# Performance work log

Measured on AMD Instinct MI355X. Metric: run time of the kernel, lower is better.

## Reference

```python
import jax, jax.numpy as jnp
import numpy as np
from jax import lax

KSIZE = 3      # match kernel
STRIDE = 1
RATE = 2       # dilation / downscale rate
FUSE_K = 3     # diagonal-fuse kernel
SCALE = 10.0   # softmax scale
FUSE = True
ESC = 1e-4     # escape_NaN, added per-element before the reduce_sum (as in torch code)


def _same_pad(x, k, s):
    # x: [C, H, W] -> zero-padded so that strided k-window 'same' extraction works
    C, H, W = x.shape
    oh, ow = -(-H // s), -(-W // s)
    ph = max(0, (oh - 1) * s + k - H)
    pw = max(0, (ow - 1) * s + k - W)
    xp = jnp.pad(x, ((0, 0), (ph // 2, ph - ph // 2), (pw // 2, pw - pw // 2)))
    return xp, oh, ow


def extract_patches(x, k, s):
    # x: [C, H, W] -> [L, C, k, k], L row-major over output grid (matches torch Unfold)
    C = x.shape[0]
    xp, oh, ow = _same_pad(x, k, s)
    cols = [xp[:, dh:dh + s * (oh - 1) + 1:s, dw:dw + s * (ow - 1) + 1:s]
            for dh in range(k) for dw in range(k)]
    p = jnp.stack(cols, 0).reshape(k, k, C, oh, ow)
    return p.transpose(3, 4, 2, 0, 1).reshape(oh * ow, C, k, k)


def fuse_diag(x):
    # conv with eye(FUSE_K) kernel, 'same' padding: sum of diagonal shifts
    A, B = x.shape
    pt = (FUSE_K - 1) // 2
    pb = FUSE_K - 1 - pt
    xp = jnp.pad(x, ((pt, pb), (pt, pb)))
    out = xp[0:A, 0:B]
    for d in range(1, FUSE_K):
        out = out + xp[d:d + A, d:d + B]
    return out


def _forward(f, b, mask):
    B, C, H, W = f.shape
    kernel = 2 * RATE
    # mask -> mm gate over background patches (shared across batch: torch uses m[0])
    mask_s = mask[0][:, ::4 * RATE, ::4 * RATE]           # [1, H/r, W/r] nearest downsample
    m = extract_patches(mask_s, KSIZE, STRIDE)            # [L, 1, k, k]
    mm = (jnp.mean(m, axis=(1, 2, 3)) == 0.0).astype(f.dtype)[:, None, None]  # [L,1,1]

    def single(fi, bi):
        # raw patches from full-res background for reconstruction: [Lb, C, 2r, 2r]
        raw_w = extract_patches(bi, kernel, RATE * STRIDE)
        # nearest 1/rate downsample
        fs = fi[:, ::RATE, ::RATE]
        bs = bi[:, ::RATE, ::RATE]
        bh, bw = bs.shape[1], bs.shape[2]
        fh, fw = fs.shape[1], fs.shape[2]
        Lb, Lf = bh * bw, fh * fw
        # match patches from downsampled background, L2-normalized per patch
        w = extract_patches(bs, KSIZE, STRIDE)                      # [Lb, C, 3, 3]
        denom = jnp.sqrt(jnp.sum(w * w + ESC, axis=(1, 2, 3), keepdims=True))
        wn = (w / denom).reshape(Lb, -1)                            # [Lb, C*9]
        # correlation = conv of fs with wn filters = patch GEMM
        fp = extract_patches(fs, KSIZE, 1).reshape(Lf, -1)          # [Lf, C*9]
        scores = wn @ fp.T                                          # [Lb, Lf]
        if FUSE:
            s = fuse_diag(scores)
            s = s.reshape(bh, bw, fh, fw).transpose(1, 0, 3, 2).reshape(Lb, Lf)
            s = fuse_diag(s)
            s = s.reshape(bw, bh, fw, fh).transpose(1, 0, 3, 2).reshape(Lb, Lf)
            scores = s
        att = scores.reshape(Lb, fh, fw) * mm
        att = jax.nn.softmax(att * SCALE, axis=0) * mm              # softmax over patches
        # conv_transpose2d(att, raw_w, stride=rate, padding=1) / 4
        rhs = jnp.flip(raw_w, (2, 3)).transpose(1, 0, 2, 3)         # [C, Lb, 2r, 2r] OIHW
        pad = kernel - 1 - 1                                        # k - 1 - torch_padding
        out = lax.conv_general_dilated(
            att[None], rhs, window_strides=(1, 1),
            padding=[(pad, pad), (pad, pad)], lhs_dilation=(RATE, RATE),
            dimension_numbers=('NCHW', 'OIHW', 'NCHW'))[0] / 4.0    # [C, H, W]
        return out

    return jax.vmap(single)(f, b)


def setup_inputs() -> dict:
    key = jax.random.key(0)
    k1, k2 = jax.random.split(key)
    B, C, H, W = 4, 128, 96, 96
    f = jax.random.normal(k1, (B, C, H, W), jnp.float32)
    b = jax.random.normal(k2, (B, C, H, W), jnp.float32)
    mask = jnp.zeros((1, 1, 4 * H, 4 * W), jnp.float32)
    mask = mask.at[:, :, 96:288, 96:288].set(1.0)
    return {"f": f, "b": b, "mask": mask}


def reference(f, b, mask):
    return _forward(f, b, mask)
```

## Files before the change

### kernel.cpp

```cpp
#include <hip/hip_runtime.h>

typedef _Float16 half8 __attribute__((ext_vector_type(8)));
typedef float floatx4 __attribute__((ext_vector_type(4)));

#define LBF 2304
#define K1  1152
#define LDK2 2304

__device__ __forceinline__ void gll16(const _Float16* g, _Float16* l) {
    __builtin_amdgcn_global_load_lds((const __attribute__((address_space(1))) void*)g,
                                     (__attribute__((address_space(3))) void*)l, 16, 0, 0);
}

__device__ __forceinline__ int dec_kc(int s) { return (s >= 0) ? s + 1 : -s - 1; }

__global__ void stage_scan(const float* __restrict__ f, const float* __restrict__ bsrc,
                           const float* __restrict__ mask,
                           float* __restrict__ ds, int* __restrict__ pos) {
    int tid = threadIdx.x;
    if (blockIdx.x < 9216) {
        long flat = (long)blockIdx.x * 256 + tid;
        int p = flat % 2304;
        long rest = flat / 2304;
        int c = rest % 128;
        int b = (rest / 128) % 4;
        int t = rest / (128 * 4);
        int pi = p / 48, pj = p % 48;
        const float* src = t ? bsrc : f;
        ds[flat] = src[(((long)b * 128 + c) * 96 + 2 * pi) * 96 + 2 * pj];
        return;
    }
    int mmb[9], loc[9]; int s = 0;
#pragma unroll
    for (int t = 0; t < 9; t++) {
        int p = tid * 9 + t;
        int pi = p / 48, pj = p % 48;
        float sm = 0.f;
#pragma unroll
        for (int u = 0; u < 3; u++)
#pragma unroll
            for (int v = 0; v < 3; v++) {
                int y = pi - 1 + u, x = pj - 1 + v;
                if ((unsigned)y < 48u && (unsigned)x < 48u)
                    sm += mask[(8 * y) * 384 + 8 * x];
            }
        int m = (sm == 0.f) ? 1 : 0;
        mmb[t] = m; loc[t] = s; s += m;
    }
    __shared__ int sh[256];
    sh[tid] = s; __syncthreads();
    for (int off = 1; off < 256; off <<= 1) {
        int v = (tid >= off) ? sh[tid - off] : 0;
        __syncthreads();
        sh[tid] += v;
        __syncthreads();
    }
    int excl = sh[tid] - s;
#pragma unroll
    for (int t = 0; t < 9; t++) {
        int e = excl + loc[t];
        pos[tid * 9 + t] = mmb[t] ? e : (-e - 1);
    }
}

__global__ void prep_fp(const float* __restrict__ ds, _Float16* __restrict__ fp) {
    int k = blockIdx.x * 128 + threadIdx.x;
    int p = blockIdx.y;
    int b = blockIdx.z;
    int c = k / 9, r = k % 9, u = r / 3, v = r % 3;
    int pi = p / 48, pj = p % 48;
    int y = pi - 1 + u, x = pj - 1 + v;
    float val = 0.f;
    if ((unsigned)y < 48u && (unsigned)x < 48u)
        val = ds[((long)(b * 128 + c)) * 2304 + y * 48 + x];
    fp[((long)b * LBF + p) * K1 + k] = (_Float16)val;
}

__global__ void prep_wn(const float* __restrict__ ds, _Float16* __restrict__ wn) {
    int p = blockIdx.x, b = blockIdx.y;
    int tid = threadIdx.x;
    int pi = p / 48, pj = p % 48;
    const float* dsb = ds + (long)(4 + b) * 128 * 2304;
    float w[9];
    float ss = 0.f;
#pragma unroll
    for (int t = 0; t < 9; t++) {
        int k = tid + t * 128;
        int c = k / 9, r = k % 9, u = r / 3, v = r % 3;
        int y = pi - 1 + u, x = pj - 1 + v;
        float val = 0.f;
        if ((unsigned)y < 48u && (unsigned)x < 48u)
            val = dsb[(long)c * 2304 + y * 48 + x];
        w[t] = val;
        ss += val * val;
    }
    for (int m = 32; m; m >>= 1) ss += __shfl_xor(ss, m);
    __shared__ float sh[2];
    if ((tid & 63) == 0) sh[tid >> 6] = ss;
    __syncthreads();
    float denom = sqrtf(sh[0] + sh[1] + 0.1152f);
    float inv = 1.f / denom;
#pragma unroll
    for (int t = 0; t < 9; t++) {
        int k = tid + t * 128;
        wn[((long)b * LBF + p) * K1 + k] = (_Float16)(w[t] * inv);
    }
}

__global__ void prep_wtc(const float* __restrict__ bsrc, const int* __restrict__ pos,
                         _Float16* __restrict__ wtc) {
    int p = blockIdx.x * 256 + threadIdx.x;
    int c = blockIdx.y;
    int b = blockIdx.z;
    int sp = pos[p];
    long base = ((long)b * 2048 + c * 16) * LDK2;
    if (sp < 0) {
        int kc = dec_kc(pos[2303]);
        int kp = (kc + 63) & ~63;
        int mo = p + sp + 1;
        if (mo < kp - kc) {
#pragma unroll
            for (int n = 0; n < 16; n++)
                wtc[base + (long)n * LDK2 + kc + mo] = (_Float16)0.f;
        }
        return;
    }
    int pi = p / 48, pj = p % 48;
    const float* src = bsrc + ((long)b * 128 + c) * 96 * 96;
#pragma unroll
    for (int u = 0; u < 4; u++) {
        int y = 2 * pi - 1 + u;
        bool yok = (unsigned)y < 96u;
#pragma unroll
        for (int v = 0; v < 4; v++) {
            int x = 2 * pj - 1 + v;
            float val = 0.f;
            if (yok && (unsigned)x < 96u) val = src[y * 96 + x];
            wtc[base + (long)(u * 4 + v) * LDK2 + sp] = (_Float16)val;
        }
    }
}

#define REGA 8192
#define REGB 4096

__global__ __launch_bounds__(512, 2)
void gemm1_8ph(const _Float16* __restrict__ A, const _Float16* __restrict__ B,
               float* __restrict__ C) {
    extern __shared__ _Float16 smem[];
    _Float16* SA = smem;
    _Float16* SB = smem + 4 * REGA;

    int bid = blockIdx.x;
    int wg = (bid & 7) * 81 + (bid >> 3);
    int z = wg / 162; int t = wg - z * 162;
    const int m0 = (t / 18) * 256, n0 = (t % 18) * 128;

    const _Float16* gA = A + (long)z * 2304 * K1 + (long)m0 * K1;
    const _Float16* gB = B + (long)z * 2304 * K1 + (long)n0 * K1;
    float* Cb = C + (long)z * 2304 * 2304;

    const int tid = threadIdx.x;
    const int wave = tid >> 6, lane = tid & 63;
    const int lm = lane & 15, q = lane >> 4;
    const int wm = wave >> 1, wn_ = wave & 1;
    const int soff = (q ^ ((lm >> 1) & 3)) * 8;
    const int srow = lane >> 2;
    const int scol = (((lane & 3) ^ ((lane >> 3) & 3))) * 8;

    floatx4 acc[4][4] = {};

    auto stA = [&](int reg, int kcol) {
        _Float16* dst = SA + reg * REGA;
        gll16(gA + (long)(wave * 32 + srow) * K1 + kcol, dst + wave * 1024);
        gll16(gA + (long)(wave * 32 + 16 + srow) * K1 + kcol, dst + wave * 1024 + 512);
    };
    auto stB = [&](int reg, int kcol) {
        gll16(gB + (long)(wave * 16 + srow) * K1 + kcol, SB + reg * REGB + wave * 512);
    };
    auto ldA = [&](int reg, int i) -> half8 {
        return *(const half8*)&SA[reg * REGA + (wm * 64 + i * 16 + lm) * 32 + soff];
    };
    auto ldB = [&](int reg, int j) -> half8 {
        return *(const half8*)&SB[reg * REGB + (wn_ * 64 + j * 16 + lm) * 32 + soff];
    };

    stA(0, 0 + scol);  stB(0, 0 + scol);
    stA(1, 32 + scol); stB(1, 32 + scol);
    stA(2, 64 + scol); stB(2, 64 + scol);
    asm volatile("s_waitcnt vmcnt(6)" ::: "memory");
    __builtin_amdgcn_s_barrier();

    for (int k = 0; k < 18; ++k) {
        const int b = k & 1;
        const int rg0 = b * 2, rg1 = rg0 + 1, og1 = (b ^ 1) * 2 + 1;
        {
            half8 af[4], bf[4];
#pragma unroll
            for (int i = 0; i < 4; ++i) af[i] = ldA(rg0, i);
#pragma unroll
            for (int j = 0; j < 4; ++j) bf[j] = ldB(rg0, j);
            if (k + 1 < 18) { int kc = (k + 1) * 64 + 32 + scol; stA(og1, kc); stB(og1, kc); }
            asm volatile("s_waitcnt vmcnt(6)" ::: "memory");
            __builtin_amdgcn_s_barrier();
            __builtin_amdgcn_s_setprio(1);
#pragma unroll
            for (int i = 0; i < 4; ++i)
#pragma unroll
                for (int j = 0; j < 4; ++j)
                    acc[i][j] = __builtin_amdgcn_mfma_f32_16x16x32_f16(af[i], bf[j], acc[i][j], 0, 0, 0);
            __builtin_amdgcn_s_setprio(0);
            __builtin_amdgcn_s_barrier();
        }
        {
            half8 af[4], bf[4];
#pragma unroll
            for (int i = 0; i < 4; ++i) af[i] = ldA(rg1, i);
#pragma unroll
            for (int j = 0; j < 4; ++j) bf[j] = ldB(rg1, j);
            if (k + 2 < 18) { int kc = (k + 2) * 64 + scol; stA(rg0, kc); stB(rg0, kc); }
            asm volatile("s_waitcnt vmcnt(6)" ::: "memory");
            __builtin_amdgcn_s_barrier();
            __builtin_amdgcn_s_setprio(1);
#pragma unroll
            for (int i = 0; i < 4; ++i)
#pragma unroll
                for (int j = 0; j < 4; ++j)
                    acc[i][j] = __builtin_amdgcn_mfma_f32_16x16x32_f16(af[i], bf[j], acc[i][j], 0, 0, 0);
            __builtin_amdgcn_s_setprio(0);
            __builtin_amdgcn_s_barrier();
        }
    }

    const int col = n0 + wn_ * 64 + lm;
#pragma unroll
    for (int i = 0; i < 4; ++i) {
        const int row = m0 + wm * 64 + i * 16 + q * 4;
#pragma unroll
        for (int j = 0; j < 4; ++j)
#pragma unroll
            for (int r = 0; r < 4; ++r)
                Cb[(long)(row + r) * 2304 + col + j * 16] = acc[i][j][r];
    }
}

__device__ __forceinline__ void gemm_compute(const _Float16* lA, const _Float16* lB,
                                             floatx4 (&acc)[4][4],
                                             int wr, int wc, int lm, int pcp) {
    half8 af[4], bf[4];
#pragma unroll
    for (int t = 0; t < 4; t++) {
        af[t] = *(const half8*)&lA[(wr * 64 + t * 16 + lm) * 64 + pcp];
        bf[t] = *(const half8*)&lB[(wc * 64 + t * 16 + lm) * 64 + pcp];
    }
#pragma unroll
    for (int i = 0; i < 4; i++)
#pragma unroll
        for (int j = 0; j < 4; j++)
            acc[i][j] = __builtin_amdgcn_mfma_f32_16x16x32_f16(af[i], bf[j], acc[i][j], 0, 0, 0);
#pragma unroll
    for (int t = 0; t < 4; t++) {
        af[t] = *(const half8*)&lA[(wr * 64 + t * 16 + lm) * 64 + (pcp ^ 32)];
        bf[t] = *(const half8*)&lB[(wc * 64 + t * 16 + lm) * 64 + (pcp ^ 32)];
    }
#pragma unroll
    for (int i = 0; i < 4; i++)
#pragma unroll
        for (int j = 0; j < 4; j++)
            acc[i][j] = __builtin_amdgcn_mfma_f32_16x16x32_f16(af[i], bf[j], acc[i][j], 0, 0, 0);
}

__global__ __launch_bounds__(256)
void gemm_nt64(const _Float16* __restrict__ A, const _Float16* __restrict__ B,
               float* __restrict__ C, int M, int N, int ldk, int swapxy,
               const int* __restrict__ Kpos, int Kstat, long sA, long sB, long sC) {
    A += blockIdx.z * sA; B += blockIdx.z * sB; C += blockIdx.z * sC;
    int K;
    if (Kpos) { int kc = dec_kc(Kpos[0]); K = (kc + 63) & ~63; }
    else K = Kstat;
    const int tid = threadIdx.x;
    const int lane = tid & 63, wave = tid >> 6;
    const int wr = wave >> 1, wc = wave & 1;
    const int bm = swapxy ? blockIdx.x : blockIdx.y;
    const int bn = swapxy ? blockIdx.y : blockIdx.x;
    const int m0 = bm * 128, n0 = bn * 128;

    __shared__ _Float16 sm[4][128 * 64];

    floatx4 acc[4][4] = {};

    const int lm = lane & 15, q = lane >> 4;
    const int pcp = (q ^ (lm & 7)) * 8;

    const int srow8 = lane >> 3;
    const int gc = ((lane & 7) ^ srow8) * 8;
    const _Float16* gA[4]; const _Float16* gB[4];
    int dOff[4];
#pragma unroll
    for (int c = 0; c < 4; c++) {
        int r = (wave * 4 + c) * 8 + srow8;
        gA[c] = A + (long)(m0 + r) * ldk + gc;
        gB[c] = B + (long)(n0 + r) * ldk + gc;
        dOff[c] = (wave * 4 + c) * 512;
    }

    if (K > 0) {
#pragma unroll
        for (int c = 0; c < 4; c++) gll16(gA[c], &sm[0][dOff[c]]);
#pragma unroll
        for (int c = 0; c < 4; c++) gll16(gB[c], &sm[1][dOff[c]]);
        __syncthreads();
        int k0 = 0, buf = 0;
        while (true) {
            int kn = k0 + 64;
            if (kn < K) {
                const int nb = (buf ^ 1) * 2;
#pragma unroll
                for (int c = 0; c < 4; c++) gll16(gA[c] + kn, &sm[nb][dOff[c]]);
#pragma unroll
                for (int c = 0; c < 4; c++) gll16(gB[c] + kn, &sm[nb + 1][dOff[c]]);
            }
            gemm_compute(sm[buf * 2], sm[buf * 2 + 1], acc, wr, wc, lm, pcp);
            __syncthreads();
            k0 = kn; buf ^= 1;
            if (k0 >= K) break;
        }
    }

    const int col = n0 + wc * 64 + lm;
    const int rowq = q * 4;
#pragma unroll
    for (int i = 0; i < 4; i++) {
        int row = m0 + wr * 64 + i * 16 + rowq;
#pragma unroll
        for (int j = 0; j < 4; j++)
#pragma unroll
            for (int r = 0; r < 4; r++)
                C[(long)(row + r) * N + col + j * 16] = acc[i][j][r];
    }
}

__global__ __launch_bounds__(256)
void fuseA(const float* __restrict__ ST, float* __restrict__ FT1) {
    int y = blockIdx.x, bb = blockIdx.y;
    const float* S = ST + (long)bb * LBF * LBF;
    float* F = FT1 + (long)bb * LBF * LBF;
    const float* r0 = S + (long)(y > 0 ? y - 1 : 0) * LBF;
    const float* r1 = S + (long)y * LBF;
    const float* r2 = S + (long)(y < LBF - 1 ? y + 1 : y) * LBF;
    float m0 = (y > 0) ? 1.f : 0.f;
    float m2 = (y < LBF - 1) ? 1.f : 0.f;
    float* o = F + (long)y * LBF;
#pragma unroll
    for (int u = 0; u < 9; u++) {
        int x = threadIdx.x + u * 256;
        float lo = (x > 0) ? m0 * r0[x - 1] : 0.f;
        float hi = (x < LBF - 1) ? m2 * r2[x + 1] : 0.f;
        o[x] = lo + r1[x] + hi;
    }
}

__global__ __launch_bounds__(256)
void fuseB_softmax(const float* __restrict__ FT1, const int* __restrict__ pos,
                   _Float16* __restrict__ attTc_g) {
    int j = blockIdx.x, bb = blockIdx.y;
    int tid = threadIdx.x;
    const float* F = FT1 + (long)bb * LBF * LBF;
    _Float16* orow = attTc_g + ((long)bb * LBF + j) * LDK2;
    int Pj = (j % 48) * 48 + j / 48;
    long roff[3]; bool jok[3];
#pragma unroll
    for (int t = 0; t < 3; t++) {
        int j2 = Pj + t - 1;
        jok[t] = (unsigned)j2 < (unsigned)LBF;
        int jc = jok[t] ? j2 : 0;
        roff[t] = (long)((jc % 48) * 48 + jc / 48) * LBF;
    }
    float v[9]; int ps[9];
    float mx = -1e30f;
#pragma unroll
    for (int u = 0; u < 9; u++) {
        int x = tid + u * 256;
        int sp = pos[x];
        ps[u] = sp;
        float xv = 0.f;
        if (sp >= 0) {
            int a = x / 48, b = x - a * 48;
            int Px = b * 48 + a;
            float acc = 0.f;
#pragma unroll
            for (int t = 0; t < 3; t++) {
                int d2 = t - 1;
                int uu = Px + d2;
                if (jok[t] && (unsigned)uu < (unsigned)LBF) {
                    int ad = a + d2;
                    int c = ((unsigned)ad < 48u) ? (x + 48 * d2)
                          : (ad == 48 ? (b + 1) : (2255 + b));
                    acc += F[roff[t] + c];
                }
            }
            xv = acc * 10.f;
        }
        v[u] = xv;
        mx = fmaxf(mx, xv);
    }
    for (int m = 32; m; m >>= 1) mx = fmaxf(mx, __shfl_xor(mx, m));
    __shared__ float sh[4], sh2[4];
    if ((tid & 63) == 0) sh[tid >> 6] = mx;
    __syncthreads();
    mx = fmaxf(fmaxf(sh[0], sh[1]), fmaxf(sh[2], sh[3]));
    float sum = 0.f;
#pragma unroll
    for (int u = 0; u < 9; u++) { v[u] = __expf(v[u] - mx); sum += v[u]; }
    for (int m = 32; m; m >>= 1) sum += __shfl_xor(sum, m);
    if ((tid & 63) == 0) sh2[tid >> 6] = sum;
    __syncthreads();
    sum = sh2[0] + sh2[1] + sh2[2] + sh2[3];
    float inv = 1.f / sum;
#pragma unroll
    for (int u = 0; u < 9; u++) {
        if (ps[u] >= 0) orow[ps[u]] = (_Float16)(v[u] * inv);
    }
    int kc = dec_kc(pos[2303]);
    int kp = (kc + 63) & ~63;
    if (tid < kp - kc) orow[kc + tid] = (_Float16)0.f;
}

__global__ void scatter_out(const float* __restrict__ MT_, float* __restrict__ out) {
    int yx = blockIdx.x * 256 + threadIdx.x;
    int c = blockIdx.y, b = blockIdx.z;
    int y = yx / 96, x = yx % 96;
    const float* Mb = MT_ + (long)b * 2048 * LBF;
    float s = 0.f;
    for (int uu = (y + 1) & 1; uu < 4; uu += 2) {
        int fi = (y + 1 - uu) >> 1;
        if ((unsigned)fi >= 48u) continue;
        for (int vv = (x + 1) & 1; vv < 4; vv += 2) {
            int fj = (x + 1 - vv) >> 1;
            if ((unsigned)fj >= 48u) continue;
            s += Mb[(long)(c * 16 + uu * 4 + vv) * LBF + fi * 48 + fj];
        }
    }
    out[(((long)b * 128 + c) * 96 + y) * 96 + x] = 0.25f * s;
}

extern "C" void kernel_launch(void* const* d_in, const int* in_sizes, int n_in,
                              void* d_out, int out_size, void* d_ws, size_t ws_size,
                              hipStream_t stream) {
    const float* f    = (const float*)d_in[0];
    const float* bsrc = (const float*)d_in[1];
    const float* mask = (const float*)d_in[2];
    float* out = (float*)d_out;

    char* ws = (char*)d_ws;
    const size_t offR1  = 84934656;
    const size_t offWn  = offR1 + 21233664;
    const size_t offWtc = offR1 + 42467328;
    const size_t offFT1 = offWtc + 37748736;
    const size_t offPos = offFT1 + 2ul * 21233664;
    const size_t NEED   = offPos + 9216;
    if (ws_size < NEED) return;

    float*    ST    = (float*)(ws + 0);
    float*    MT    = (float*)(ws + 0);
    _Float16* fp    = (_Float16*)(ws + offR1);
    _Float16* wn    = (_Float16*)(ws + offWn);
    _Float16* attTc = (_Float16*)(ws + offR1);
    _Float16* Wtc   = (_Float16*)(ws + offWtc);
    float*    ds    = (float*)(ws + offFT1);
    float*    FT1   = (float*)(ws + offFT1);
    int*      pos   = (int*)(ws + offPos);

    stage_scan<<<dim3(9217), 256, 0, stream>>>(f, bsrc, mask, ds, pos);
    prep_fp<<<dim3(9, 2304, 4), 128, 0, stream>>>(ds, fp);
    prep_wn<<<dim3(2304, 4), 128, 0, stream>>>(ds, wn);
    prep_wtc<<<dim3(9, 128, 4), 256, 0, stream>>>(bsrc, pos, Wtc);

    hipFuncSetAttribute((const void*)gemm1_8ph,
                        hipFuncAttributeMaxDynamicSharedMemorySize, 98304);
    gemm1_8ph<<<dim3(648), 512, 98304, stream>>>(fp, wn, ST);

    for (int g = 0; g < 2; g++) {
        fuseA<<<dim3(LBF, 2), 256, 0, stream>>>(ST + (long)g * 2 * LBF * LBF, FT1);
        fuseB_softmax<<<dim3(LBF, 2), 256, 0, stream>>>(FT1, pos,
            attTc + (long)g * 2 * LBF * LDK2);
    }

    gemm_nt64<<<dim3(16, 18, 4), 256, 0, stream>>>(Wtc, attTc, MT, 2048, 2304, LDK2, 1,
        pos + 2303, 0, (long)2048 * LDK2, (long)2304 * LDK2, (long)2048 * 2304);

    scatter_out<<<dim3(36, 128, 4), 256, 0, stream>>>(MT, out);
}
```

Before: 468.2 us.

## Fuse diagonal-fuse passes into softmax kernel and shrink first GEMM tile

```diff
diff --git a/kernel.cpp b/kernel.cpp
--- a/kernel.cpp
+++ b/kernel.cpp
@@ -141,24 +141,22 @@
     }
 }
 
-#define REGA 8192
-#define REGB 4096
-
-__global__ __launch_bounds__(512, 2)
-void gemm1_8ph(const _Float16* __restrict__ A, const _Float16* __restrict__ B,
-               float* __restrict__ C) {
-    extern __shared__ _Float16 smem[];
-    _Float16* SA = smem;
-    _Float16* SB = smem + 4 * REGA;
+#define G1_REG 4096
+
+__global__ __launch_bounds__(256)
+void gemm1_cv(const _Float16* __restrict__ A, const _Float16* __restrict__ B,
+              float* __restrict__ C) {
+    __shared__ _Float16 SA[4 * G1_REG];
+    __shared__ _Float16 SB[4 * G1_REG];
 
     int bid = blockIdx.x;
-    int wg = (bid & 7) * 81 + (bid >> 3);
-    int z = wg / 162; int t = wg - z * 162;
-    const int m0 = (t / 18) * 256, n0 = (t % 18) * 128;
-
-    const _Float16* gA = A + (long)z * 2304 * K1 + (long)m0 * K1;
-    const _Float16* gB = B + (long)z * 2304 * K1 + (long)n0 * K1;
-    float* Cb = C + (long)z * 2304 * 2304;
+    int wg = (bid & 7) * 162 + (bid >> 3);
+    int z = wg / 324; int t = wg - z * 324;
+    const int m0 = (t / 18) * 128, n0 = (t % 18) * 128;
+
+    const _Float16* gA = A + (long)z * LBF * K1 + (long)m0 * K1;
+    const _Float16* gB = B + (long)z * LBF * K1 + (long)n0 * K1;
+    float* Cb = C + (long)z * LBF * LBF;
 
     const int tid = threadIdx.x;
     const int wave = tid >> 6, lane = tid & 63;
@@ -166,29 +164,31 @@
     const int wm = wave >> 1, wn_ = wave & 1;
     const int soff = (q ^ ((lm >> 1) & 3)) * 8;
     const int srow = lane >> 2;
-    const int scol = (((lane & 3) ^ ((lane >> 3) & 3))) * 8;
+    const int scol = ((lane & 3) ^ ((lane >> 3) & 3)) * 8;
 
     floatx4 acc[4][4] = {};
 
     auto stA = [&](int reg, int kcol) {
-        _Float16* dst = SA + reg * REGA;
-        gll16(gA + (long)(wave * 32 + srow) * K1 + kcol, dst + wave * 1024);
-        gll16(gA + (long)(wave * 32 + 16 + srow) * K1 + kcol, dst + wave * 1024 + 512);
+        _Float16* dst = SA + reg * G1_REG + wave * 1024;
+        gll16(gA + (long)(wave * 32 + srow) * K1 + kcol + scol, dst);
+        gll16(gA + (long)(wave * 32 + 16 + srow) * K1 + kcol + scol, dst + 512);
     };
     auto stB = [&](int reg, int kcol) {
-        gll16(gB + (long)(wave * 16 + srow) * K1 + kcol, SB + reg * REGB + wave * 512);
+        _Float16* dst = SB + reg * G1_REG + wave * 1024;
+        gll16(gB + (long)(wave * 32 + srow) * K1 + kcol + scol, dst);
+        gll16(gB + (long)(wave * 32 + 16 + srow) * K1 + kcol + scol, dst + 512);
     };
     auto ldA = [&](int reg, int i) -> half8 {
-        return *(const half8*)&SA[reg * REGA + (wm * 64 + i * 16 + lm) * 32 + soff];
+        return *(const half8*)&SA[reg * G1_REG + (wm * 64 + i * 16 + lm) * 32 + soff];
     };
     auto ldB = [&](int reg, int j) -> half8 {
-        return *(const half8*)&SB[reg * REGB + (wn_ * 64 + j * 16 + lm) * 32 + soff];
+        return *(const half8*)&SB[reg * G1_REG + (wn_ * 64 + j * 16 + lm) * 32 + soff];
     };
 
-    stA(0, 0 + scol);  stB(0, 0 + scol);
-    stA(1, 32 + scol); stB(1, 32 + scol);
-    stA(2, 64 + scol); stB(2, 64 + scol);
-    asm volatile("s_waitcnt vmcnt(6)" ::: "memory");
+    stA(0, 0);  stB(0, 0);
+    stA(1, 32); stB(1, 32);
+    stA(2, 64); stB(2, 64);
+    asm volatile("s_waitcnt vmcnt(8)" ::: "memory");
     __builtin_amdgcn_s_barrier();
 
     for (int k = 0; k < 18; ++k) {
@@ -200,9 +200,15 @@
             for (int i = 0; i < 4; ++i) af[i] = ldA(rg0, i);
 #pragma unroll
             for (int j = 0; j < 4; ++j) bf[j] = ldB(rg0, j);
-            if (k + 1 < 18) { int kc = (k + 1) * 64 + 32 + scol; stA(og1, kc); stB(og1, kc); }
-            asm volatile("s_waitcnt vmcnt(6)" ::: "memory");
+            if (k + 1 < 18) {
+                int kc = (k + 1) * 64 + 32;
+                stA(og1, kc); stB(og1, kc);
+                asm volatile("s_waitcnt vmcnt(8) lgkmcnt(0)" ::: "memory");
+            } else {
+                asm volatile("s_waitcnt vmcnt(0) lgkmcnt(0)" ::: "memory");
+            }
             __builtin_amdgcn_s_barrier();
+            __builtin_amdgcn_sched_barrier(0);
             __builtin_amdgcn_s_setprio(1);
 #pragma unroll
             for (int i = 0; i < 4; ++i)
@@ -210,6 +216,7 @@
                 for (int j = 0; j < 4; ++j)
                     acc[i][j] = __builtin_amdgcn_mfma_f32_16x16x32_f16(af[i], bf[j], acc[i][j], 0, 0, 0);
             __builtin_amdgcn_s_setprio(0);
+            __builtin_amdgcn_sched_barrier(0);
             __builtin_amdgcn_s_barrier();
         }
         {
@@ -218,9 +225,15 @@
             for (int i = 0; i < 4; ++i) af[i] = ldA(rg1, i);
 #pragma unroll
             for (int j = 0; j < 4; ++j) bf[j] = ldB(rg1, j);
-            if (k + 2 < 18) { int kc = (k + 2) * 64 + scol; stA(rg0, kc); stB(rg0, kc); }
-            asm volatile("s_waitcnt vmcnt(6)" ::: "memory");
+            if (k + 2 < 18) {
+                int kc = (k + 2) * 64;
+                stA(rg0, kc); stB(rg0, kc);
+                asm volatile("s_waitcnt vmcnt(8) lgkmcnt(0)" ::: "memory");
+            } else {
+                asm volatile("s_waitcnt vmcnt(0) lgkmcnt(0)" ::: "memory");
+            }
             __builtin_amdgcn_s_barrier();
+            __builtin_amdgcn_sched_barrier(0);
             __builtin_amdgcn_s_setprio(1);
 #pragma unroll
             for (int i = 0; i < 4; ++i)
@@ -228,6 +241,7 @@
                 for (int j = 0; j < 4; ++j)
                     acc[i][j] = __builtin_amdgcn_mfma_f32_16x16x32_f16(af[i], bf[j], acc[i][j], 0, 0, 0);
             __builtin_amdgcn_s_setprio(0);
+            __builtin_amdgcn_sched_barrier(0);
             __builtin_amdgcn_s_barrier();
         }
     }
@@ -240,7 +254,7 @@
         for (int j = 0; j < 4; ++j)
 #pragma unroll
             for (int r = 0; r < 4; ++r)
-                Cb[(long)(row + r) * 2304 + col + j * 16] = acc[i][j][r];
+                Cb[(long)(row + r) * LBF + col + j * 16] = acc[i][j][r];
     }
 }
 
@@ -341,40 +355,20 @@
 }
 
 __global__ __launch_bounds__(256)
-void fuseA(const float* __restrict__ ST, float* __restrict__ FT1) {
-    int y = blockIdx.x, bb = blockIdx.y;
-    const float* S = ST + (long)bb * LBF * LBF;
-    float* F = FT1 + (long)bb * LBF * LBF;
-    const float* r0 = S + (long)(y > 0 ? y - 1 : 0) * LBF;
-    const float* r1 = S + (long)y * LBF;
-    const float* r2 = S + (long)(y < LBF - 1 ? y + 1 : y) * LBF;
-    float m0 = (y > 0) ? 1.f : 0.f;
-    float m2 = (y < LBF - 1) ? 1.f : 0.f;
-    float* o = F + (long)y * LBF;
-#pragma unroll
-    for (int u = 0; u < 9; u++) {
-        int x = threadIdx.x + u * 256;
-        float lo = (x > 0) ? m0 * r0[x - 1] : 0.f;
-        float hi = (x < LBF - 1) ? m2 * r2[x + 1] : 0.f;
-        o[x] = lo + r1[x] + hi;
-    }
-}
-
-__global__ __launch_bounds__(256)
-void fuseB_softmax(const float* __restrict__ FT1, const int* __restrict__ pos,
-                   _Float16* __restrict__ attTc_g) {
+void fuse_sm(const float* __restrict__ ST, const int* __restrict__ pos,
+             _Float16* __restrict__ attTc_g) {
     int j = blockIdx.x, bb = blockIdx.y;
     int tid = threadIdx.x;
-    const float* F = FT1 + (long)bb * LBF * LBF;
+    const float* S = ST + (long)bb * LBF * LBF;
     _Float16* orow = attTc_g + ((long)bb * LBF + j) * LDK2;
     int Pj = (j % 48) * 48 + j / 48;
-    long roff[3]; bool jok[3];
+    int Rr[3]; bool jok[3];
 #pragma unroll
     for (int t = 0; t < 3; t++) {
         int j2 = Pj + t - 1;
         jok[t] = (unsigned)j2 < (unsigned)LBF;
         int jc = jok[t] ? j2 : 0;
-        roff[t] = (long)((jc % 48) * 48 + jc / 48) * LBF;
+        Rr[t] = (jc % 48) * 48 + jc / 48;
     }
     float v[9]; int ps[9];
     float mx = -1e30f;
@@ -386,17 +380,22 @@
         float xv = 0.f;
         if (sp >= 0) {
             int a = x / 48, b = x - a * 48;
-            int Px = b * 48 + a;
             float acc = 0.f;
 #pragma unroll
             for (int t = 0; t < 3; t++) {
                 int d2 = t - 1;
-                int uu = Px + d2;
+                int uu = b * 48 + a + d2;
                 if (jok[t] && (unsigned)uu < (unsigned)LBF) {
                     int ad = a + d2;
                     int c = ((unsigned)ad < 48u) ? (x + 48 * d2)
                           : (ad == 48 ? (b + 1) : (2255 + b));
-                    acc += F[roff[t] + c];
+                    int R = Rr[t];
+#pragma unroll
+                    for (int e = -1; e <= 1; ++e) {
+                        int rr = R + e, cc = c + e;
+                        if ((unsigned)rr < (unsigned)LBF && (unsigned)cc < (unsigned)LBF)
+                            acc += S[(long)rr * LBF + cc];
+                    }
                 }
             }
             xv = acc * 10.f;
@@ -468,7 +467,6 @@
     _Float16* attTc = (_Float16*)(ws + offR1);
     _Float16* Wtc   = (_Float16*)(ws + offWtc);
     float*    ds    = (float*)(ws + offFT1);
-    float*    FT1   = (float*)(ws + offFT1);
     int*      pos   = (int*)(ws + offPos);
 
     stage_scan<<<dim3(9217), 256, 0, stream>>>(f, bsrc, mask, ds, pos);
@@ -476,15 +474,9 @@
     prep_wn<<<dim3(2304, 4), 128, 0, stream>>>(ds, wn);
     prep_wtc<<<dim3(9, 128, 4), 256, 0, stream>>>(bsrc, pos, Wtc);
 
-    hipFuncSetAttribute((const void*)gemm1_8ph,
-                        hipFuncAttributeMaxDynamicSharedMemorySize, 98304);
-    gemm1_8ph<<<dim3(648), 512, 98304, stream>>>(fp, wn, ST);
-
-    for (int g = 0; g < 2; g++) {
-        fuseA<<<dim3(LBF, 2), 256, 0, stream>>>(ST + (long)g * 2 * LBF * LBF, FT1);
-        fuseB_softmax<<<dim3(LBF, 2), 256, 0, stream>>>(FT1, pos,
-            attTc + (long)g * 2 * LBF * LDK2);
-    }
+    gemm1_cv<<<dim3(1296), 256, 0, stream>>>(fp, wn, ST);
+
+    fuse_sm<<<dim3(LBF, 4), 256, 0, stream>>>(ST, pos, attTc);
 
     gemm_nt64<<<dim3(16, 18, 4), 256, 0, stream>>>(Wtc, attTc, MT, 2048, 2304, LDK2, 1,
         pos + 2303, 0, (long)2048 * LDK2, (long)2304 * LDK2, (long)2048 * 2304);
```

New measurement: 484.9 us. +3.6%, slower.
